# Performance work log

Measured on AMD Instinct MI355X. Metric: run time of the kernel, lower is better.

Reference implementation:

```python
import jax, jax.numpy as jnp
import numpy as np

GAMMA = 1.0

def setup_inputs() -> dict:
    key = jax.random.key(0)
    k1, k2 = jax.random.split(key)
    source_features = jax.random.normal(k1, (4096, 2048), dtype=jnp.float32)
    target_features = jax.random.normal(k2, (4096, 2048), dtype=jnp.float32)
    return {"source_features": source_features, "target_features": target_features}

def _gaussian_kernel_mean(x, y, gamma):
    # Original: ((x_i - y_j)**2).mean(-1) / D  == sqdist_ij / D**2
    # Computed via the x^2 + y^2 - 2xy GEMM trick instead of tiling O(N*M*D).
    d = x.shape[1]
    x2 = jnp.sum(x * x, axis=1)  # [N]
    y2 = jnp.sum(y * y, axis=1)  # [M]
    xy = x @ y.T                 # [N, M]
    sqdist = x2[:, None] + y2[None, :] - 2.0 * xy
    k = jnp.exp(-gamma * sqdist / (d * d))
    return jnp.mean(k)

def reference(source_features, target_features):
    source = source_features.reshape(source_features.shape[0], -1)
    target = target_features.reshape(target_features.shape[0], -1)
    # Equal batch sizes -> padding branch in the original is a no-op.
    xx = _gaussian_kernel_mean(source, source, GAMMA)
    yy = _gaussian_kernel_mean(target, target, GAMMA)
    xy = _gaussian_kernel_mean(source, target, GAMMA)
    return xx + yy - 2.0 * xy
```

## Files before the change

kernel.cpp:

```cpp
#include <hip/hip_runtime.h>
#include <stdint.h>
#include <stddef.h>

#define AS1 __attribute__((address_space(1)))
#define AS3 __attribute__((address_space(3)))

typedef short bf16x8 __attribute__((ext_vector_type(8)));
typedef float f32x4 __attribute__((ext_vector_type(4)));
typedef unsigned short u16x8 __attribute__((ext_vector_type(8)));

static constexpr int N = 4096;
static constexpr int K = 2048;
static constexpr int BM = 128;
static constexpr int TILES = N / BM;
static constexpr int NBLK = TILES * TILES;

__device__ __forceinline__ unsigned short f2bf(float f) {
  union { float f; uint32_t u; } v; v.f = f;
  return (unsigned short)((v.u + 0x7FFFu + ((v.u >> 16) & 1u)) >> 16);
}

__global__ __launch_bounds__(256) void prep_kernel(
    const float* __restrict__ X, const float* __restrict__ Y,
    float* __restrict__ x2, float* __restrict__ y2,
    unsigned short* __restrict__ Xb, unsigned short* __restrict__ Yb, int wb) {
  const int row = blockIdx.x;
  const float* src = blockIdx.y ? Y : X;
  float* nrm = blockIdx.y ? y2 : x2;
  unsigned short* dst = blockIdx.y ? Yb : Xb;
  const size_t base = (size_t)row * K + threadIdx.x * 8;
  const float4 a = *(const float4*)(src + base);
  const float4 b = *(const float4*)(src + base + 4);
  double s = (double)a.x * a.x + (double)a.y * a.y + (double)a.z * a.z +
             (double)a.w * a.w + (double)b.x * b.x + (double)b.y * b.y +
             (double)b.z * b.z + (double)b.w * b.w;
  if (wb) {
    u16x8 o;
    o[0] = f2bf(a.x); o[1] = f2bf(a.y); o[2] = f2bf(a.z); o[3] = f2bf(a.w);
    o[4] = f2bf(b.x); o[5] = f2bf(b.y); o[6] = f2bf(b.z); o[7] = f2bf(b.w);
    *(u16x8*)(dst + base) = o;
  }
#pragma unroll
  for (int off = 32; off; off >>= 1) s += __shfl_down(s, off);
  __shared__ double red[4];
  if ((threadIdx.x & 63) == 0) red[threadIdx.x >> 6] = s;
  __syncthreads();
  if (threadIdx.x == 0) nrm[row] = (float)(red[0] + red[1] + red[2] + red[3]);
}


#define RB3(bb, o) ((unsigned)((bb)*32768u + (o)*16384u))
#define VM2 asm volatile("s_waitcnt vmcnt(2)" ::: "memory")
#define LGKM0                                                                  \
  do {                                                                         \
    asm volatile("s_waitcnt lgkmcnt(0)" ::: "memory");                         \
    __builtin_amdgcn_sched_barrier(0);                                         \
  } while (0)

#define STG(O, TT, BB, H)                                                      \
  do {                                                                         \
    const unsigned short* _sp = (O) ? Bpan : Apan;                             \
    const unsigned int _so =                                                   \
        ((O) ? sB : sA) + (unsigned)(H) * 262144u + (unsigned)(TT) * 64u;      \
    const unsigned int _lb = RB3(BB, O) + (unsigned)(H) * 8192u + wseg;        \
    __builtin_amdgcn_global_load_lds(                                          \
        (const AS1 unsigned int*)(_sp + _so),                                  \
        (AS3 unsigned int*)(lds + _lb), 16, 0, 0);                             \
    __builtin_amdgcn_global_load_lds(                                          \
        (const AS1 unsigned int*)(_sp + _so + 16384u),                         \
        (AS3 unsigned int*)(lds + _lb + 512u), 16, 0, 0);                      \
  } while (0)

#define RDA(KS, BB)                                                            \
  _Pragma("unroll") for (int _mi = 0; _mi < 8; ++_mi)                          \
      af[_mi] = *(const bf16x8*)(lds + RB3(BB, 0) + (aoff[_mi] ^ ((KS) * 32u)))

#define RDB(VAR, IDX, KS, BB)                                                  \
  VAR = *(const bf16x8*)(lds + RB3(BB, 1) + (boff[IDX] ^ ((KS) * 32u)))

#define MFMA_P(X0, X1, C0, C1)                                                 \
  do {                                                                         \
    __builtin_amdgcn_s_setprio(1);                                             \
    _Pragma("unroll") for (int _mi = 0; _mi < 8; ++_mi) {                      \
      acc[_mi][C0] = __builtin_amdgcn_mfma_f32_16x16x32_bf16(                  \
          af[_mi], X0, acc[_mi][C0], 0, 0, 0);                                 \
      acc[_mi][C1] = __builtin_amdgcn_mfma_f32_16x16x32_bf16(                  \
          af[_mi], X1, acc[_mi][C1], 0, 0, 0);                                 \
    }                                                                          \
    __builtin_amdgcn_s_setprio(0);                                             \
  } while (0)

#define TILE4(T, BB)                                                           \
  do {                                                                         \
    const int _t1 = ((T) + 1 < 32) ? (T) + 1 : 31;                             \
    const int _t2 = ((T) + 2 < 32) ? (T) + 2 : 31;                             \
                                                               \
    LGKM0; MFMA_P(b0, b1, 0, 1);                                               \
    RDB(b2, 2, 0, BB); RDB(b3, 3, 0, BB);                                      \
    STG(0, _t1, 1 - (BB), 1);                                                  \
    __builtin_amdgcn_s_barrier();                                              \
                                                               \
    LGKM0; MFMA_P(b2, b3, 2, 3);                                               \
    RDA(1, BB); RDB(b0, 0, 1, BB); RDB(b1, 1, 1, BB);                          \
    STG(1, _t1, 1 - (BB), 0);                                                  \
    __builtin_amdgcn_s_barrier();                                              \
                                                               \
    LGKM0; MFMA_P(b0, b1, 0, 1);                                               \
    RDB(b2, 2, 1, BB); RDB(b3, 3, 1, BB);                                      \
    STG(1, _t1, 1 - (BB), 1);                                                  \
    __builtin_amdgcn_s_barrier();                                              \
                                                               \
    LGKM0; MFMA_P(b2, b3, 2, 3);                                               \
    STG(0, _t2, (BB), 0);                                                      \
    VM2;                                                                       \
    RDA(0, 1 - (BB)); RDB(b0, 0, 0, 1 - (BB)); RDB(b1, 1, 0, 1 - (BB));        \
    __builtin_amdgcn_s_barrier();                                              \
  } while (0)

__global__ __launch_bounds__(512, 2) void mmd_gemm8(
    const unsigned short* __restrict__ Xb, const unsigned short* __restrict__ Yb,
    const float* __restrict__ x2, const float* __restrict__ y2,
    double* __restrict__ partials) {
  __shared__ __align__(16) unsigned short lds[65536];

  const int bid = blockIdx.x;
  const int logical = (bid & 7) * 62 + (bid >> 3);
  int ti, tj;
  const unsigned short *Apan, *Bpan;
  const float *rn, *cn;
  double wgt;
  if (logical < 256) {
    ti = logical & 15; tj = logical >> 4;
    Apan = Xb; Bpan = Yb; rn = x2; cn = y2; wgt = -2.0;
  } else {
    const int q = logical - 256;
    const int pp = q / 120;
    int jj = q % 120;
    int rr = 0;
    while (jj >= 15 - rr) { jj -= 15 - rr; ++rr; }
    ti = rr; tj = rr + 1 + jj;
    Apan = Bpan = pp ? Yb : Xb;
    rn = cn = pp ? y2 : x2;
    wgt = 2.0;
  }
  const int i0 = ti << 8, j0 = tj << 8;

  const int tid = threadIdx.x;
  const int w = tid >> 6, l = tid & 63;
  const int wm = w >> 2, wn = w & 3;
  const int lr = l & 15, lq = l >> 4;

  const int ci = w * 128 + l;
  const int rr0 = ci >> 3;
  const int cc0 = (ci & 7) ^ (rr0 & 7);
  const unsigned int sA = (unsigned)(i0 + rr0) * (unsigned)K + (unsigned)(cc0 * 8);
  const unsigned int sB = (unsigned)(j0 + rr0) * (unsigned)K + (unsigned)(cc0 * 8);
  const unsigned int wseg = (unsigned)w * 1024u;

  unsigned int aoff[8], boff[4];
#pragma unroll
  for (int mi = 0; mi < 8; ++mi) {
    const int r = wm * 128 + mi * 16 + lr;
    aoff[mi] = (unsigned)(r * 64 + ((lq ^ (r & 7)) * 8));
  }
#pragma unroll
  for (int ni = 0; ni < 4; ++ni) {
    const int rb = wn * 64 + ni * 16 + lr;
    boff[ni] = (unsigned)(rb * 64 + ((lq ^ (rb & 7)) * 8));
  }

  f32x4 acc[8][4] = {};
  bf16x8 af[8], b0, b1, b2, b3;

  STG(0, 0, 0, 0); STG(0, 0, 0, 1); STG(1, 0, 0, 0); STG(1, 0, 0, 1);
  STG(0, 1, 1, 0);
  VM2;
  __builtin_amdgcn_s_barrier();
  RDA(0, 0); RDB(b0, 0, 0, 0); RDB(b1, 1, 0, 0);

#pragma unroll 1
  for (int tt = 0; tt < 32; tt += 2) {
    TILE4(tt, 0);
    TILE4(tt + 1, 1);
  }

  const float ce = -1.0f / (2048.0f * 2048.0f);
  double s = 0.0;
#pragma unroll
  for (int mi = 0; mi < 8; ++mi) {
#pragma unroll
    for (int r4 = 0; r4 < 4; ++r4) {
      const float rv = rn[i0 + wm * 128 + mi * 16 + lq * 4 + r4];
#pragma unroll
      for (int ni = 0; ni < 4; ++ni) {
        const float cv = cn[j0 + wn * 64 + ni * 16 + lr];
        const float tx = ce * (rv + cv - 2.0f * acc[mi][ni][r4]);
        const float v =
            tx * (1.0f + tx * (0.5f + tx * (0.16666667f + tx * 0.041666668f)));
        s += (double)v;
      }
    }
  }
#pragma unroll
  for (int off = 32; off; off >>= 1) s += __shfl_down(s, off);
  __shared__ double red[8];
  if (l == 0) red[w] = s;
  __syncthreads();
  if (tid == 0) {
    double tot = 0.0;
#pragma unroll
    for (int i = 0; i < 8; ++i) tot += red[i];
    partials[logical] = wgt * tot;
  }
}

__global__ __launch_bounds__(256) void mmd_sym128(
    const unsigned short* __restrict__ Xb, const unsigned short* __restrict__ Yb,
    const float* __restrict__ x2, const float* __restrict__ y2,
    double* __restrict__ partials) {
  const int bid = blockIdx.x;
  const int logical = (bid & 7) * 12 + (bid >> 3);
  const int p = logical / 48;
  const int r2_ = logical % 48;
  const int d = r2_ / 3;
  const int sub = r2_ % 3;
  const double wgt = (sub == 1) ? 2.0 : 1.0;

  const unsigned short* Pan = p ? Yb : Xb;
  const float* nrm = p ? y2 : x2;
  const int i0 = d * 256 + ((sub == 2) ? 128 : 0);
  const int j0 = d * 256 + ((sub >= 1) ? 128 : 0);

  __shared__ __align__(16) unsigned short As[128 * 64];
  __shared__ __align__(16) unsigned short Bs[128 * 64];

  const int tid = threadIdx.x;
  const int w = tid >> 6, l = tid & 63;
  const int m_base = (w >> 1) * 64, n_base = (w & 1) * 64;
  const int lr = l & 15, lq = l >> 4;

  f32x4 acc[4][4] = {};

  for (int k0 = 0; k0 < K; k0 += 64) {
#pragma unroll
    for (int u = 0; u < 4; ++u) {
      const int seg = w * 4 + u;
      const int f = seg * 64 + l;
      const int row = f >> 3;
      const int scol = ((f & 7) ^ (row & 7)) * 8;
      __builtin_amdgcn_global_load_lds(
          (const AS1 unsigned int*)(Pan + (size_t)(i0 + row) * K + k0 + scol),
          (AS3 unsigned int*)(As + seg * 512), 16, 0, 0);
      __builtin_amdgcn_global_load_lds(
          (const AS1 unsigned int*)(Pan + (size_t)(j0 + row) * K + k0 + scol),
          (AS3 unsigned int*)(Bs + seg * 512), 16, 0, 0);
    }
    __syncthreads();

#pragma unroll
    for (int kk = 0; kk < 64; kk += 32) {
      bf16x8 af2[4], bfr[4];
      const int ch = (kk >> 3) + lq;
#pragma unroll
      for (int mi = 0; mi < 4; ++mi) {
        const int r = m_base + mi * 16 + lr;
        af2[mi] = *(const bf16x8*)((const char*)As + r * 128 + ((ch ^ (r & 7)) * 16));
      }
#pragma unroll
      for (int ni = 0; ni < 4; ++ni) {
        const int r = n_base + ni * 16 + lr;
        bfr[ni] = *(const bf16x8*)((const char*)Bs + r * 128 + ((ch ^ (r & 7)) * 16));
      }
#pragma unroll
      for (int mi = 0; mi < 4; ++mi)
#pragma unroll
        for (int ni = 0; ni < 4; ++ni)
          acc[mi][ni] = __builtin_amdgcn_mfma_f32_16x16x32_bf16(
              af2[mi], bfr[ni], acc[mi][ni], 0, 0, 0);
    }
    __syncthreads();
  }

  const float ce = -1.0f / (2048.0f * 2048.0f);
  double s = 0.0;
#pragma unroll
  for (int mi = 0; mi < 4; ++mi) {
#pragma unroll
    for (int r4 = 0; r4 < 4; ++r4) {
      const float rv = nrm[i0 + m_base + mi * 16 + lq * 4 + r4];
#pragma unroll
      for (int ni = 0; ni < 4; ++ni) {
        const float cv = nrm[j0 + n_base + ni * 16 + lr];
        const float tx = ce * (rv + cv - 2.0f * acc[mi][ni][r4]);
        const float v =
            tx * (1.0f + tx * (0.5f + tx * (0.16666667f + tx * 0.041666668f)));
        s += (double)v;
      }
    }
  }
#pragma unroll
  for (int off = 32; off; off >>= 1) s += __shfl_down(s, off);
  __shared__ double red[4];
  if (l == 0) red[w] = s;
  __syncthreads();
  if (tid == 0)
    partials[496 + logical] = wgt * (red[0] + red[1] + red[2] + red[3]);
}

__global__ __launch_bounds__(256) void mmd_gemm_f32(
    const float* __restrict__ Xp, const float* __restrict__ Yp,
    const float* __restrict__ x2, const float* __restrict__ y2,
    double* __restrict__ partials) {
  const int p = blockIdx.y;
  const float* Ap = (p == 1) ? Yp : Xp;
  const float* Bp = (p == 0) ? Xp : Yp;
  const float* rn = (p == 1) ? y2 : x2;
  const float* cn = (p == 0) ? x2 : y2;
  const double wgt = (p == 2) ? -2.0 : 1.0;

  const int bx = blockIdx.x;
  const int i0 = (bx & (TILES - 1)) * BM;
  const int j0 = (bx / TILES) * BM;

  __shared__ __align__(16) unsigned short As[BM * 64];
  __shared__ __align__(16) unsigned short Bs[BM * 64];

  const int tid = threadIdx.x;
  const int w = tid >> 6, l = tid & 63;
  const int m_base = (w >> 1) * 64, n_base = (w & 1) * 64;

  f32x4 acc[4][4] = {};

  for (int k0 = 0; k0 < K; k0 += 64) {
#pragma unroll
    for (int u = 0; u < 4; ++u) {
      const int f = u * 256 + tid;
      const int row = f >> 3;
      const int cir = f & 7;
      const int dstb = row * 128 + ((cir ^ (row & 7)) * 16);
      {
        const float* g = Ap + (size_t)(i0 + row) * K + k0 + cir * 8;
        const float4 v0 = *(const float4*)g;
        const float4 v1 = *(const float4*)(g + 4);
        u16x8 o;
        o[0] = f2bf(v0.x); o[1] = f2bf(v0.y); o[2] = f2bf(v0.z); o[3] = f2bf(v0.w);
        o[4] = f2bf(v1.x); o[5] = f2bf(v1.y); o[6] = f2bf(v1.z); o[7] = f2bf(v1.w);
        *(u16x8*)((char*)As + dstb) = o;
      }
      {
        const float* g = Bp + (size_t)(j0 + row) * K + k0 + cir * 8;
        const float4 v0 = *(const float4*)g;
        const float4 v1 = *(const float4*)(g + 4);
        u16x8 o;
        o[0] = f2bf(v0.x); o[1] = f2bf(v0.y); o[2] = f2bf(v0.z); o[3] = f2bf(v0.w);
        o[4] = f2bf(v1.x); o[5] = f2bf(v1.y); o[6] = f2bf(v1.z); o[7] = f2bf(v1.w);
        *(u16x8*)((char*)Bs + dstb) = o;
      }
    }
    __syncthreads();

#pragma unroll
    for (int kk = 0; kk < 64; kk += 32) {
      bf16x8 af2[4], bfr[4];
      const int lr = l & 15;
      const int ch = (kk >> 3) + (l >> 4);
#pragma unroll
      for (int mi = 0; mi < 4; ++mi) {
        const int r = m_base + mi * 16 + lr;
        af2[mi] = *(const bf16x8*)((const char*)As + r * 128 + ((ch ^ (r & 7)) * 16));
      }
#pragma unroll
      for (int ni = 0; ni < 4; ++ni) {
        const int r = n_base + ni * 16 + lr;
        bfr[ni] = *(const bf16x8*)((const char*)Bs + r * 128 + ((ch ^ (r & 7)) * 16));
      }
#pragma unroll
      for (int mi = 0; mi < 4; ++mi)
#pragma unroll
        for (int ni = 0; ni < 4; ++ni)
          acc[mi][ni] = __builtin_amdgcn_mfma_f32_16x16x32_bf16(
              af2[mi], bfr[ni], acc[mi][ni], 0, 0, 0);
    }
    __syncthreads();
  }

  const float ce = -1.0f / (2048.0f * 2048.0f);
  double s = 0.0;
  const int lr = l & 15, lq = l >> 4;
#pragma unroll
  for (int mi = 0; mi < 4; ++mi) {
#pragma unroll
    for (int r4 = 0; r4 < 4; ++r4) {
      const float rv = rn[i0 + m_base + mi * 16 + lq * 4 + r4];
#pragma unroll
      for (int ni = 0; ni < 4; ++ni) {
        const float cv = cn[j0 + n_base + ni * 16 + lr];
        const float tx = ce * (rv + cv - 2.0f * acc[mi][ni][r4]);
        const float v =
            tx * (1.0f + tx * (0.5f + tx * (0.16666667f + tx * 0.041666668f)));
        s += (double)v;
      }
    }
  }
#pragma unroll
  for (int off = 32; off; off >>= 1) s += __shfl_down(s, off);
  __shared__ double red[4];
  if (l == 0) red[w] = s;
  __syncthreads();
  if (tid == 0) partials[p * NBLK + bx] = wgt * (red[0] + red[1] + red[2] + red[3]);
}

__global__ __launch_bounds__(256) void finalize_kernel(
    const double* __restrict__ partials, float* __restrict__ out, int n) {
  double s = 0.0;
  for (int i = threadIdx.x; i < n; i += 256) s += partials[i];
#pragma unroll
  for (int off = 32; off; off >>= 1) s += __shfl_down(s, off);
  __shared__ double red[4];
  if ((threadIdx.x & 63) == 0) red[threadIdx.x >> 6] = s;
  __syncthreads();
  if (threadIdx.x == 0)
    out[0] = (float)((red[0] + red[1] + red[2] + red[3]) *
                     (1.0 / ((double)N * (double)N)));
}

extern "C" void kernel_launch(void* const* d_in, const int* in_sizes, int n_in,
                              void* d_out, int out_size, void* d_ws,
                              size_t ws_size, hipStream_t stream) {
  const float* X = (const float*)d_in[0];
  const float* Y = (const float*)d_in[1];
  char* ws = (char*)d_ws;

  double* partials = (double*)ws;
  float* x2 = (float*)(ws + 24576);
  float* y2 = (float*)(ws + 24576 + 16384);
  unsigned short* Xb = (unsigned short*)(ws + 65536);
  unsigned short* Yb = Xb + (size_t)N * K;
  const size_t need_fast = (size_t)65536 + (size_t)2 * N * K * 2;
  const bool fast = ws_size >= need_fast;

  prep_kernel<<<dim3(N, 2), 256, 0, stream>>>(X, Y, x2, y2, Xb, Yb, fast ? 1 : 0);
  if (fast) {
    mmd_gemm8<<<dim3(496), dim3(512), 0, stream>>>(Xb, Yb, x2, y2, partials);
    mmd_sym128<<<dim3(96), dim3(256), 0, stream>>>(Xb, Yb, x2, y2, partials);
    finalize_kernel<<<1, 256, 0, stream>>>(partials, (float*)d_out, 592);
  } else {
    mmd_gemm_f32<<<dim3(NBLK, 3), 256, 0, stream>>>(X, Y, x2, y2, partials);
    finalize_kernel<<<1, 256, 0, stream>>>(partials, (float*)d_out, 3072);
  }
}
```

Baseline: 175.0 us.

## Fuse diagonal 128-tile kernel into main GEMM launch and rebalance stage loads

Merges the separate diagonal-block kernel into the main 256x256 GEMM kernel as extra blocks (592 total), so the diagonal tiles run alongside the off-diagonal tiles instead of in a second, under-filled launch. The diagonal path is rewritten for 512 threads using the shared LDS buffer. It also moves one global-to-LDS staging load earlier in the TILE4 pipeline, spreading the loads differently across the barriers. This removes one launch and its tail, but the small-tile blocks now run under the big kernel's 512-thread, large-LDS occupancy limits and may land on the critical path.

```diff
diff --git a/kernel.cpp b/kernel.cpp
--- a/kernel.cpp
+++ b/kernel.cpp
@@ -97,17 +97,16 @@
                                                                \
     LGKM0; MFMA_P(b0, b1, 0, 1);                                               \
     RDB(b2, 2, 0, BB); RDB(b3, 3, 0, BB);                                      \
-    STG(0, _t1, 1 - (BB), 1);                                                  \
+    STG(0, _t1, 1 - (BB), 1); STG(1, _t1, 1 - (BB), 0);                        \
     __builtin_amdgcn_s_barrier();                                              \
                                                                \
     LGKM0; MFMA_P(b2, b3, 2, 3);                                               \
     RDA(1, BB); RDB(b0, 0, 1, BB); RDB(b1, 1, 1, BB);                          \
-    STG(1, _t1, 1 - (BB), 0);                                                  \
+    STG(1, _t1, 1 - (BB), 1);                                                  \
     __builtin_amdgcn_s_barrier();                                              \
                                                                \
     LGKM0; MFMA_P(b0, b1, 0, 1);                                               \
     RDB(b2, 2, 1, BB); RDB(b3, 3, 1, BB);                                      \
-    STG(1, _t1, 1 - (BB), 1);                                                  \
     __builtin_amdgcn_s_barrier();                                              \
                                                                \
     LGKM0; MFMA_P(b2, b3, 2, 3);                                               \
@@ -122,189 +121,183 @@
     const float* __restrict__ x2, const float* __restrict__ y2,
     double* __restrict__ partials) {
   __shared__ __align__(16) unsigned short lds[65536];
+  __shared__ double red[8];
 
   const int bid = blockIdx.x;
-  const int logical = (bid & 7) * 62 + (bid >> 3);
-  int ti, tj;
-  const unsigned short *Apan, *Bpan;
-  const float *rn, *cn;
-  double wgt;
-  if (logical < 256) {
-    ti = logical & 15; tj = logical >> 4;
-    Apan = Xb; Bpan = Yb; rn = x2; cn = y2; wgt = -2.0;
-  } else {
-    const int q = logical - 256;
-    const int pp = q / 120;
-    int jj = q % 120;
-    int rr = 0;
-    while (jj >= 15 - rr) { jj -= 15 - rr; ++rr; }
-    ti = rr; tj = rr + 1 + jj;
-    Apan = Bpan = pp ? Yb : Xb;
-    rn = cn = pp ? y2 : x2;
-    wgt = 2.0;
-  }
-  const int i0 = ti << 8, j0 = tj << 8;
-
   const int tid = threadIdx.x;
   const int w = tid >> 6, l = tid & 63;
-  const int wm = w >> 2, wn = w & 3;
   const int lr = l & 15, lq = l >> 4;
-
-  const int ci = w * 128 + l;
-  const int rr0 = ci >> 3;
-  const int cc0 = (ci & 7) ^ (rr0 & 7);
-  const unsigned int sA = (unsigned)(i0 + rr0) * (unsigned)K + (unsigned)(cc0 * 8);
-  const unsigned int sB = (unsigned)(j0 + rr0) * (unsigned)K + (unsigned)(cc0 * 8);
-  const unsigned int wseg = (unsigned)w * 1024u;
-
-  unsigned int aoff[8], boff[4];
-#pragma unroll
-  for (int mi = 0; mi < 8; ++mi) {
-    const int r = wm * 128 + mi * 16 + lr;
-    aoff[mi] = (unsigned)(r * 64 + ((lq ^ (r & 7)) * 8));
+  const float ce = -1.0f / (2048.0f * 2048.0f);
+
+  if (bid < 496) {
+    const int logical = (bid & 7) * 62 + (bid >> 3);
+    int ti, tj;
+    const unsigned short *Apan, *Bpan;
+    const float *rn, *cn;
+    double wgt;
+    if (logical < 256) {
+      ti = logical & 15; tj = logical >> 4;
+      Apan = Xb; Bpan = Yb; rn = x2; cn = y2; wgt = -2.0;
+    } else {
+      const int q = logical - 256;
+      const int pp = q / 120;
+      int jj = q % 120;
+      int rr = 0;
+      while (jj >= 15 - rr) { jj -= 15 - rr; ++rr; }
+      ti = rr; tj = rr + 1 + jj;
+      Apan = Bpan = pp ? Yb : Xb;
+      rn = cn = pp ? y2 : x2;
+      wgt = 2.0;
+    }
+    const int i0 = ti << 8, j0 = tj << 8;
+    const int wm = w >> 2, wn = w & 3;
+
+    const int ci = w * 128 + l;
+    const int rr0 = ci >> 3;
+    const int cc0 = (ci & 7) ^ (rr0 & 7);
+    const unsigned int sA = (unsigned)(i0 + rr0) * (unsigned)K + (unsigned)(cc0 * 8);
+    const unsigned int sB = (unsigned)(j0 + rr0) * (unsigned)K + (unsigned)(cc0 * 8);
+    const unsigned int wseg = (unsigned)w * 1024u;
+
+    unsigned int aoff[8], boff[4];
+#pragma unroll
+    for (int mi = 0; mi < 8; ++mi) {
+      const int r = wm * 128 + mi * 16 + lr;
+      aoff[mi] = (unsigned)(r * 64 + ((lq ^ (r & 7)) * 8));
+    }
+#pragma unroll
+    for (int ni = 0; ni < 4; ++ni) {
+      const int rb = wn * 64 + ni * 16 + lr;
+      boff[ni] = (unsigned)(rb * 64 + ((lq ^ (rb & 7)) * 8));
+    }
+
+    f32x4 acc[8][4] = {};
+    bf16x8 af[8], b0, b1, b2, b3;
+
+    STG(0, 0, 0, 0); STG(0, 0, 0, 1); STG(1, 0, 0, 0); STG(1, 0, 0, 1);
+    STG(0, 1, 1, 0);
+    VM2;
+    __builtin_amdgcn_s_barrier();
+    RDA(0, 0); RDB(b0, 0, 0, 0); RDB(b1, 1, 0, 0);
+
+#pragma unroll 1
+    for (int tt = 0; tt < 32; tt += 2) {
+      TILE4(tt, 0);
+      TILE4(tt + 1, 1);
+    }
+
+    double s = 0.0;
+#pragma unroll
+    for (int mi = 0; mi < 8; ++mi) {
+#pragma unroll
+      for (int r4 = 0; r4 < 4; ++r4) {
+        const float rv = rn[i0 + wm * 128 + mi * 16 + lq * 4 + r4];
+#pragma unroll
+        for (int ni = 0; ni < 4; ++ni) {
+          const float cv = cn[j0 + wn * 64 + ni * 16 + lr];
+          const float tx = ce * (rv + cv - 2.0f * acc[mi][ni][r4]);
+          const float v =
+              tx * (1.0f + tx * (0.5f + tx * (0.16666667f + tx * 0.041666668f)));
+          s += (double)v;
+        }
+      }
+    }
+#pragma unroll
+    for (int off = 32; off; off >>= 1) s += __shfl_down(s, off);
+    if (l == 0) red[w] = s;
+    __syncthreads();
+    if (tid == 0) {
+      double tot = 0.0;
+#pragma unroll
+      for (int i = 0; i < 8; ++i) tot += red[i];
+      partials[logical] = wgt * tot;
+    }
+  } else {
+    const int lg2 = ((bid - 496) & 7) * 12 + ((bid - 496) >> 3);
+    const int p = lg2 / 48;
+    const int rem = lg2 % 48;
+    const int d = rem / 3, sub = rem % 3;
+    const double wgt = (sub == 1) ? 2.0 : 1.0;
+    const unsigned short* Pan = p ? Yb : Xb;
+    const float* nrm = p ? y2 : x2;
+    const int i0 = d * 256 + ((sub == 2) ? 128 : 0);
+    const int j0 = d * 256 + ((sub >= 1) ? 128 : 0);
+
+    const int m_b = (w >> 2) * 64, n_b = (w & 3) * 32;
+
+    const int ci0l = w * 64 + l, ci1l = ci0l + 512;
+    const int rA0 = ci0l >> 3, cA0 = (ci0l & 7) ^ (rA0 & 7);
+    const int rA1 = ci1l >> 3, cA1 = (ci1l & 7) ^ (rA1 & 7);
+    const unsigned int sLA0 = (unsigned)(i0 + rA0) * K + (unsigned)(cA0 * 8);
+    const unsigned int sLA1 = (unsigned)(i0 + rA1) * K + (unsigned)(cA1 * 8);
+    const unsigned int sLB0 = (unsigned)(j0 + rA0) * K + (unsigned)(cA0 * 8);
+    const unsigned int sLB1 = (unsigned)(j0 + rA1) * K + (unsigned)(cA1 * 8);
+    const unsigned int d0 = (unsigned)w * 512u, d1 = 4096u + (unsigned)w * 512u;
+
+    f32x4 acc2[4][2] = {};
+
+#pragma unroll 1
+    for (int k0 = 0; k0 < K; k0 += 64) {
+      __builtin_amdgcn_global_load_lds((const AS1 unsigned int*)(Pan + sLA0 + k0),
+                                       (AS3 unsigned int*)(lds + d0), 16, 0, 0);
+      __builtin_amdgcn_global_load_lds((const AS1 unsigned int*)(Pan + sLA1 + k0),
+                                       (AS3 unsigned int*)(lds + d1), 16, 0, 0);
+      __builtin_amdgcn_global_load_lds((const AS1 unsigned int*)(Pan + sLB0 + k0),
+                                       (AS3 unsigned int*)(lds + 8192u + d0), 16, 0, 0);
+      __builtin_amdgcn_global_load_lds((const AS1 unsigned int*)(Pan + sLB1 + k0),
+                                       (AS3 unsigned int*)(lds + 8192u + d1), 16, 0, 0);
+      __syncthreads();
+#pragma unroll
+      for (int kk = 0; kk < 64; kk += 32) {
+        const int ch = (kk >> 3) + lq;
+        bf16x8 a2[4], bb[2];
+#pragma unroll
+        for (int mi = 0; mi < 4; ++mi) {
+          const int r = m_b + mi * 16 + lr;
+          a2[mi] = *(const bf16x8*)(lds + r * 64 + ((ch ^ (r & 7)) * 8));
+        }
+#pragma unroll
+        for (int ni = 0; ni < 2; ++ni) {
+          const int r = n_b + ni * 16 + lr;
+          bb[ni] = *(const bf16x8*)(lds + 8192 + r * 64 + ((ch ^ (r & 7)) * 8));
+        }
+#pragma unroll
+        for (int mi = 0; mi < 4; ++mi)
+#pragma unroll
+          for (int ni = 0; ni < 2; ++ni)
+            acc2[mi][ni] = __builtin_amdgcn_mfma_f32_16x16x32_bf16(
+                a2[mi], bb[ni], acc2[mi][ni], 0, 0, 0);
+      }
+      __syncthreads();
+    }
+
+    double s = 0.0;
+#pragma unroll
+    for (int mi = 0; mi < 4; ++mi) {
+#pragma unroll
+      for (int r4 = 0; r4 < 4; ++r4) {
+        const float rv = nrm[i0 + m_b + mi * 16 + lq * 4 + r4];
+#pragma unroll
+        for (int ni = 0; ni < 2; ++ni) {
+          const float cv = nrm[j0 + n_b + ni * 16 + lr];
+          const float tx = ce * (rv + cv - 2.0f * acc2[mi][ni][r4]);
+          const float v =
+              tx * (1.0f + tx * (0.5f + tx * (0.16666667f + tx * 0.041666668f)));
+          s += (double)v;
+        }
+      }
+    }
+#pragma unroll
+    for (int off = 32; off; off >>= 1) s += __shfl_down(s, off);
+    if (l == 0) red[w] = s;
+    __syncthreads();
+    if (tid == 0) {
+      double tot = 0.0;
+#pragma unroll
+      for (int i = 0; i < 8; ++i) tot += red[i];
+      partials[496 + lg2] = wgt * tot;
+    }
   }
-#pragma unroll
-  for (int ni = 0; ni < 4; ++ni) {
-    const int rb = wn * 64 + ni * 16 + lr;
-    boff[ni] = (unsigned)(rb * 64 + ((lq ^ (rb & 7)) * 8));
-  }
-
-  f32x4 acc[8][4] = {};
-  bf16x8 af[8], b0, b1, b2, b3;
-
-  STG(0, 0, 0, 0); STG(0, 0, 0, 1); STG(1, 0, 0, 0); STG(1, 0, 0, 1);
-  STG(0, 1, 1, 0);
-  VM2;
-  __builtin_amdgcn_s_barrier();
-  RDA(0, 0); RDB(b0, 0, 0, 0); RDB(b1, 1, 0, 0);
-
-#pragma unroll 1
-  for (int tt = 0; tt < 32; tt += 2) {
-    TILE4(tt, 0);
-    TILE4(tt + 1, 1);
-  }
-
-  const float ce = -1.0f / (2048.0f * 2048.0f);
-  double s = 0.0;
-#pragma unroll
-  for (int mi = 0; mi < 8; ++mi) {
-#pragma unroll
-    for (int r4 = 0; r4 < 4; ++r4) {
-      const float rv = rn[i0 + wm * 128 + mi * 16 + lq * 4 + r4];
-#pragma unroll
-      for (int ni = 0; ni < 4; ++ni) {
-        const float cv = cn[j0 + wn * 64 + ni * 16 + lr];
-        const float tx = ce * (rv + cv - 2.0f * acc[mi][ni][r4]);
-        const float v =
-            tx * (1.0f + tx * (0.5f + tx * (0.16666667f + tx * 0.041666668f)));
-        s += (double)v;
-      }
-    }
-  }
-#pragma unroll
-  for (int off = 32; off; off >>= 1) s += __shfl_down(s, off);
-  __shared__ double red[8];
-  if (l == 0) red[w] = s;
-  __syncthreads();
-  if (tid == 0) {
-    double tot = 0.0;
-#pragma unroll
-    for (int i = 0; i < 8; ++i) tot += red[i];
-    partials[logical] = wgt * tot;
-  }
-}
-
-__global__ __launch_bounds__(256) void mmd_sym128(
-    const unsigned short* __restrict__ Xb, const unsigned short* __restrict__ Yb,
-    const float* __restrict__ x2, const float* __restrict__ y2,
-    double* __restrict__ partials) {
-  const int bid = blockIdx.x;
-  const int logical = (bid & 7) * 12 + (bid >> 3);
-  const int p = logical / 48;
-  const int r2_ = logical % 48;
-  const int d = r2_ / 3;
-  const int sub = r2_ % 3;
-  const double wgt = (sub == 1) ? 2.0 : 1.0;
-
-  const unsigned short* Pan = p ? Yb : Xb;
-  const float* nrm = p ? y2 : x2;
-  const int i0 = d * 256 + ((sub == 2) ? 128 : 0);
-  const int j0 = d * 256 + ((sub >= 1) ? 128 : 0);
-
-  __shared__ __align__(16) unsigned short As[128 * 64];
-  __shared__ __align__(16) unsigned short Bs[128 * 64];
-
-  const int tid = threadIdx.x;
-  const int w = tid >> 6, l = tid & 63;
-  const int m_base = (w >> 1) * 64, n_base = (w & 1) * 64;
-  const int lr = l & 15, lq = l >> 4;
-
-  f32x4 acc[4][4] = {};
-
-  for (int k0 = 0; k0 < K; k0 += 64) {
-#pragma unroll
-    for (int u = 0; u < 4; ++u) {
-      const int seg = w * 4 + u;
-      const int f = seg * 64 + l;
-      const int row = f >> 3;
-      const int scol = ((f & 7) ^ (row & 7)) * 8;
-      __builtin_amdgcn_global_load_lds(
-          (const AS1 unsigned int*)(Pan + (size_t)(i0 + row) * K + k0 + scol),
-          (AS3 unsigned int*)(As + seg * 512), 16, 0, 0);
-      __builtin_amdgcn_global_load_lds(
-          (const AS1 unsigned int*)(Pan + (size_t)(j0 + row) * K + k0 + scol),
-          (AS3 unsigned int*)(Bs + seg * 512), 16, 0, 0);
-    }
-    __syncthreads();
-
-#pragma unroll
-    for (int kk = 0; kk < 64; kk += 32) {
-      bf16x8 af2[4], bfr[4];
-      const int ch = (kk >> 3) + lq;
-#pragma unroll
-      for (int mi = 0; mi < 4; ++mi) {
-        const int r = m_base + mi * 16 + lr;
-        af2[mi] = *(const bf16x8*)((const char*)As + r * 128 + ((ch ^ (r & 7)) * 16));
-      }
-#pragma unroll
-      for (int ni = 0; ni < 4; ++ni) {
-        const int r = n_base + ni * 16 + lr;
-        bfr[ni] = *(const bf16x8*)((const char*)Bs + r * 128 + ((ch ^ (r & 7)) * 16));
-      }
-#pragma unroll
-      for (int mi = 0; mi < 4; ++mi)
-#pragma unroll
-        for (int ni = 0; ni < 4; ++ni)
-          acc[mi][ni] = __builtin_amdgcn_mfma_f32_16x16x32_bf16(
-              af2[mi], bfr[ni], acc[mi][ni], 0, 0, 0);
-    }
-    __syncthreads();
-  }
-
-  const float ce = -1.0f / (2048.0f * 2048.0f);
-  double s = 0.0;
-#pragma unroll
-  for (int mi = 0; mi < 4; ++mi) {
-#pragma unroll
-    for (int r4 = 0; r4 < 4; ++r4) {
-      const float rv = nrm[i0 + m_base + mi * 16 + lq * 4 + r4];
-#pragma unroll
-      for (int ni = 0; ni < 4; ++ni) {
-        const float cv = nrm[j0 + n_base + ni * 16 + lr];
-        const float tx = ce * (rv + cv - 2.0f * acc[mi][ni][r4]);
-        const float v =
-            tx * (1.0f + tx * (0.5f + tx * (0.16666667f + tx * 0.041666668f)));
-        s += (double)v;
-      }
-    }
-  }
-#pragma unroll
-  for (int off = 32; off; off >>= 1) s += __shfl_down(s, off);
-  __shared__ double red[4];
-  if (l == 0) red[w] = s;
-  __syncthreads();
-  if (tid == 0)
-    partials[496 + logical] = wgt * (red[0] + red[1] + red[2] + red[3]);
 }
 
 __global__ __launch_bounds__(256) void mmd_gemm_f32(
@@ -441,8 +434,7 @@
 
   prep_kernel<<<dim3(N, 2), 256, 0, stream>>>(X, Y, x2, y2, Xb, Yb, fast ? 1 : 0);
   if (fast) {
-    mmd_gemm8<<<dim3(496), dim3(512), 0, stream>>>(Xb, Yb, x2, y2, partials);
-    mmd_sym128<<<dim3(96), dim3(256), 0, stream>>>(Xb, Yb, x2, y2, partials);
+    mmd_gemm8<<<dim3(592), dim3(512), 0, stream>>>(Xb, Yb, x2, y2, partials);
     finalize_kernel<<<1, 256, 0, stream>>>(partials, (float*)d_out, 592);
   } else {
     mmd_gemm_f32<<<dim3(NBLK, 3), 256, 0, stream>>>(X, Y, x2, y2, partials);
```

Measured after the change: 166.7 us. -4.7%, faster.
